# Optimization experiments

Hardware: AMD Instinct MI355X
Metric: run time of the kernel (lower is better)

Reference implementation:

```python
import jax, jax.numpy as jnp
import numpy as np

B, S, H, DH = 1, 4096, 8, 40  # hardcoded in the original forward
D = H * DH  # 320

def setup_inputs() -> dict:
    key = jax.random.key(0)
    ks = jax.random.split(key, 6)
    s = 1.0 / np.sqrt(D)
    return {
        "x": jax.random.normal(ks[0], (B, S, D), dtype=jnp.float32),
        "Wq": jax.random.normal(ks[1], (D, D), dtype=jnp.float32) * s,
        "Wk": jax.random.normal(ks[2], (D, D), dtype=jnp.float32) * s,
        "Wv": jax.random.normal(ks[3], (D, D), dtype=jnp.float32) * s,
        "Wo": jax.random.normal(ks[4], (D, D), dtype=jnp.float32) * s,
        "bo": jnp.zeros((D,), dtype=jnp.float32),
    }

def reference(x, Wq, Wk, Wv, Wo, bo):
    scale = DH ** (-0.5)
    # nn.Linear(bias=False): y = x @ W^T. context = x (self-attention).
    q = x @ Wq.T
    k = x @ Wk.T
    v = x @ Wv.T
    # split heads: [B,S,D] -> [B*H, S, DH]
    def split_heads(t):
        return t.reshape(B, S, H, DH).transpose(0, 2, 1, 3).reshape(B * H, S, DH)
    q, k, v = split_heads(q), split_heads(k), split_heads(v)
    # fp32 QK^T (original forces float), softmax, AV
    sim = jnp.einsum('bid,bjd->bij', q.astype(jnp.float32), k.astype(jnp.float32)) * scale
    attn = jax.nn.softmax(sim, axis=-1)
    out = jnp.einsum('bij,bjd->bid', attn, v)
    # merge heads: [B*H, S, DH] -> [B, S, D]
    out = out.reshape(B, H, S, DH).transpose(0, 2, 1, 3).reshape(B, S, D)
    return out @ Wo.T + bo
```

## Files before the change

### kernel.cpp

```cpp
#include <hip/hip_runtime.h>
#include <math.h>


#define NS 4096
#define ND 320
#define SCALE2 0.2281101152f
#define HS48 196608
#define VTH 163840
#define XN 1310720

typedef __attribute__((ext_vector_type(8))) short bf16x8;
typedef __attribute__((ext_vector_type(16))) float f32x16;

static __device__ __forceinline__ unsigned short f2bru(float f) {
  return (unsigned short)((__builtin_bit_cast(unsigned int, f) + 0x8000u) >> 16);
}
static __device__ __forceinline__ unsigned int pk2ru(float a, float b) {
  unsigned int ua = __builtin_bit_cast(unsigned int, a) + 0x8000u;
  unsigned int ub = __builtin_bit_cast(unsigned int, b) + 0x8000u;
  return __builtin_amdgcn_perm(ub, ua, 0x07060302u);
}
static __device__ __forceinline__ unsigned int pk2t(float a, float b) {
  return __builtin_amdgcn_perm(__builtin_bit_cast(unsigned int, b),
                               __builtin_bit_cast(unsigned int, a), 0x07060302u);
}
static __device__ __forceinline__ float fexp2(float x) {
  return __builtin_amdgcn_exp2f(x);
}
static __device__ __forceinline__ bf16x8 ld8(const unsigned short* p) {
  union { uint2 u[2]; bf16x8 v; } c;
  c.u[0] = *(const uint2*)p;
  c.u[1] = *(const uint2*)(p + 4);
  return c.v;
}
static __device__ __forceinline__ uint4 ld16u(const unsigned short* p) {
  uint2 a = *(const uint2*)p, b = *(const uint2*)(p + 4);
  return make_uint4(a.x, a.y, b.x, b.y);
}
static __device__ __forceinline__ void st16(unsigned short* p, uint4 v) {
  *(uint2*)p = make_uint2(v.x, v.y);
  *(uint2*)(p + 4) = make_uint2(v.z, v.w);
}
static __device__ __forceinline__ int sig32(int q) {
  int s = q >> 4, h2 = (q >> 3) & 1, j = q & 7;
  return (s << 4) | ((j >> 2) << 3) | (h2 << 2) | (j & 3);
}

__global__ __launch_bounds__(256) void proj_qkv_kernel(
    const float* __restrict__ x, const float* __restrict__ Wq,
    const float* __restrict__ Wk, const float* __restrict__ Wv,
    unsigned short* __restrict__ Qp, unsigned short* __restrict__ Kp,
    unsigned short* __restrict__ Vt) {
  const int zi = blockIdx.y;
  const int z = zi / 5;
  const int bnn = (zi - z * 5) * 64;
  const float* W = (z == 0) ? Wq : (z == 1) ? Wk : Wv;
  __shared__ __align__(16) unsigned short As[128 * 76];
  __shared__ __align__(16) unsigned short Bs[64 * 76];
  const int t = threadIdx.x;
  const int w = t >> 6, l = t & 63, l31 = l & 31, hi = l >> 5;
  const int bm = blockIdx.x * 128;
  const int m0 = w * 32;
  f32x16 acc0 = {0,0,0,0,0,0,0,0,0,0,0,0,0,0,0,0};
  f32x16 acc1 = {0,0,0,0,0,0,0,0,0,0,0,0,0,0,0,0};
  const unsigned short* af = As + (m0 + l31) * 76 + hi * 8;
  const unsigned short* bf0 = Bs + l31 * 76 + hi * 8;
  const unsigned short* bf1 = Bs + (32 + l31) * 76 + hi * 8;
  for (int k0 = 0; k0 < ND; k0 += 64) {
    __syncthreads();
#pragma unroll
    for (int i = 0; i < 4; i++) {
      int c = t + i * 256;
      int row = c >> 3, kc = (c & 7) << 3;
      const float* g = x + (bm + row) * ND + k0 + kc;
      float4 v0 = *(const float4*)g, v1 = *(const float4*)(g + 4);
      st16(As + row * 76 + kc,
           make_uint4(pk2ru(v0.x, v0.y), pk2ru(v0.z, v0.w),
                      pk2ru(v1.x, v1.y), pk2ru(v1.z, v1.w)));
    }
#pragma unroll
    for (int i = 0; i < 2; i++) {
      int c = t + i * 256;
      int row = c >> 3, kc = (c & 7) << 3;
      const float* g = W + (bnn + row) * ND + k0 + kc;
      float4 v0 = *(const float4*)g, v1 = *(const float4*)(g + 4);
      st16(Bs + row * 76 + kc,
           make_uint4(pk2ru(v0.x, v0.y), pk2ru(v0.z, v0.w),
                      pk2ru(v1.x, v1.y), pk2ru(v1.z, v1.w)));
    }
    __syncthreads();
#pragma unroll
    for (int ks = 0; ks < 4; ks++) {
      bf16x8 A = ld8(af + ks * 16);
      acc0 = __builtin_amdgcn_mfma_f32_32x32x16_bf16(A, ld8(bf0 + ks * 16), acc0, 0, 0, 0);
      acc1 = __builtin_amdgcn_mfma_f32_32x32x16_bf16(A, ld8(bf1 + ks * 16), acc1, 0, 0, 0);
    }
  }
  __syncthreads();
  if (z < 2) {
    unsigned short* Tile = As;
    unsigned short* Y = (z == 0) ? Qp : Kp;
    const float sc = (z == 0) ? SCALE2 : 1.0f;
    const unsigned int padw = (z == 0) ? 0xC200u : 0x3F80u;
#pragma unroll
    for (int r2 = 0; r2 < 16; r2++) {
      int lr = m0 + (r2 & 3) + 8 * (r2 >> 2) + 4 * hi;
      Tile[lr * 68 + l31] = f2bru(acc0[r2] * sc);
      Tile[lr * 68 + 32 + l31] = f2bru(acc1[r2] * sc);
    }
    __syncthreads();
#pragma unroll
    for (int i = 0; i < 4; i++) {
      int c = t + i * 256;
      int row = c >> 3, ch = c & 7;
      int j = bnn + ch * 8;
      int h = j / 40, dh = j - h * 40;
      uint4 v = ld16u(Tile + row * 68 + ch * 8);
      st16(Y + h * HS48 + (bm + row) * 48 + dh, v);
      if (dh == 0)
        st16(Y + h * HS48 + (bm + row) * 48 + 40, make_uint4(padw, 0u, 0u, 0u));
    }
  } else {
    unsigned short* Tile = As;
#pragma unroll
    for (int r2 = 0; r2 < 16; r2++) {
      int lr = m0 + (r2 & 3) + 8 * (r2 >> 2) + 4 * hi;
      Tile[l31 * 132 + lr] = f2bru(acc0[r2]);
      Tile[(32 + l31) * 132 + lr] = f2bru(acc1[r2]);
    }
    __syncthreads();
#pragma unroll
    for (int i = 0; i < 4; i++) {
      int c = t + i * 256;
      int row = c >> 4, ch = c & 15;
      int j = bnn + row;
      int h = j / 40, dd = j - h * 40;
      uint4 v = ld16u(Tile + row * 132 + ch * 8);
      st16(Vt + h * VTH + dd * NS + bm + ch * 8, v);
    }
  }
}

__global__ __launch_bounds__(256) void attn_kernel(
    const unsigned short* __restrict__ Qp, const unsigned short* __restrict__ Kp,
    const unsigned short* __restrict__ Vt, unsigned short* __restrict__ Op,
    float* __restrict__ Lp) {
  const int b = blockIdx.x;
  const int h = b & 7, ks = (b >> 3) & 7, qt = b >> 6;
  const int t = threadIdx.x;
  const int w = t >> 6, l = t & 63, l31 = l & 31, hi = l >> 5;
  __shared__ __align__(16) unsigned short Ks[64 * 68];
  __shared__ __align__(16) unsigned short Vs[48 * 68];
  for (int i = t; i < 272; i += 256)
    ((unsigned int*)(Vs + 40 * 68))[i] = (i < 34) ? 0x3F803F80u : 0u;

  const int kbase = ks * 512;
  const int qbase = qt * 128 + w * 32;
  const unsigned short* qp = Qp + h * HS48 + (qbase + l31) * 48 + hi * 8;
  bf16x8 qf0 = *(const bf16x8*)qp;
  bf16x8 qf1 = *(const bf16x8*)(qp + 16);
  bf16x8 qf2 = *(const bf16x8*)(qp + 32);

  f32x16 oa0 = {0,0,0,0,0,0,0,0,0,0,0,0,0,0,0,0};
  f32x16 oa1 = {0,0,0,0,0,0,0,0,0,0,0,0,0,0,0,0};

  const int kr0 = t / 6, kc0 = t - kr0 * 6;
  const int kr1 = (t + 256) / 6, kc1 = (t + 256) - kr1 * 6;
  const unsigned short* gK0 = Kp + h * HS48 + (kbase + kr0) * 48 + kc0 * 8;
  const unsigned short* gK1 = Kp + h * HS48 + (kbase + kr1) * 48 + kc1 * 8;
  unsigned short* lK0 = Ks + ((kr0 & 32) | sig32(kr0 & 31)) * 68 + kc0 * 8;
  unsigned short* lK1 = Ks + ((kr1 & 32) | sig32(kr1 & 31)) * 68 + kc1 * 8;
  const int vr0 = t >> 3, vc = t & 7, vr1 = 32 + vr0;
  const unsigned short* gV0 = Vt + h * VTH + vr0 * NS + kbase + vc * 8;
  const unsigned short* gV1 = Vt + h * VTH + vr1 * NS + kbase + vc * 8;
  unsigned short* lV0 = Vs + vr0 * 68 + vc * 8;
  unsigned short* lV1 = Vs + vr1 * 68 + vc * 8;

  const unsigned short* kf0 = Ks + l31 * 68 + hi * 8;
  const unsigned short* kf1 = Ks + (32 + l31) * 68 + hi * 8;
  const unsigned short* vf0 = Vs + l31 * 68 + hi * 8;
  const unsigned short* vf1 = Vs + (32 + (l31 & 15)) * 68 + hi * 8;

  uint4 ka = *(const uint4*)gK0;
  uint4 kb2, vb2;
  uint4 va = *(const uint4*)gV0;
  if (t < 128) kb2 = *(const uint4*)gK1;
  if (t < 64)  vb2 = *(const uint4*)gV1;

  for (int it = 0; it < 8; ++it) {
    __syncthreads();
    st16(lK0, ka);
    if (t < 128) st16(lK1, kb2);
    st16(lV0, va);
    if (t < 64) st16(lV1, vb2);
    __syncthreads();
    gK0 += 64 * 48; gK1 += 64 * 48; gV0 += 64; gV1 += 64;
    ka = *(const uint4*)gK0;
    va = *(const uint4*)gV0;
    if (t < 128) kb2 = *(const uint4*)gK1;
    if (t < 64)  vb2 = *(const uint4*)gV1;

    {
      f32x16 s0 = {0,0,0,0,0,0,0,0,0,0,0,0,0,0,0,0};
      s0 = __builtin_amdgcn_mfma_f32_32x32x16_bf16(ld8(kf0), qf0, s0, 0, 0, 0);
      s0 = __builtin_amdgcn_mfma_f32_32x32x16_bf16(ld8(kf0 + 16), qf1, s0, 0, 0, 0);
      s0 = __builtin_amdgcn_mfma_f32_32x32x16_bf16(ld8(kf0 + 32), qf2, s0, 0, 0, 0);
      unsigned int pw[8];
#pragma unroll
      for (int i = 0; i < 8; i++)
        pw[i] = pk2t(fexp2(s0[2 * i]), fexp2(s0[2 * i + 1]));
      bf16x8 pf0 = __builtin_bit_cast(bf16x8, make_uint4(pw[0], pw[1], pw[2], pw[3]));
      bf16x8 pf1 = __builtin_bit_cast(bf16x8, make_uint4(pw[4], pw[5], pw[6], pw[7]));
      oa0 = __builtin_amdgcn_mfma_f32_32x32x16_bf16(pf0, ld8(vf0), oa0, 0, 0, 0);
      oa1 = __builtin_amdgcn_mfma_f32_32x32x16_bf16(pf0, ld8(vf1), oa1, 0, 0, 0);
      oa0 = __builtin_amdgcn_mfma_f32_32x32x16_bf16(pf1, ld8(vf0 + 16), oa0, 0, 0, 0);
      oa1 = __builtin_amdgcn_mfma_f32_32x32x16_bf16(pf1, ld8(vf1 + 16), oa1, 0, 0, 0);
    }
    {
      f32x16 s1 = {0,0,0,0,0,0,0,0,0,0,0,0,0,0,0,0};
      s1 = __builtin_amdgcn_mfma_f32_32x32x16_bf16(ld8(kf1), qf0, s1, 0, 0, 0);
      s1 = __builtin_amdgcn_mfma_f32_32x32x16_bf16(ld8(kf1 + 16), qf1, s1, 0, 0, 0);
      s1 = __builtin_amdgcn_mfma_f32_32x32x16_bf16(ld8(kf1 + 32), qf2, s1, 0, 0, 0);
      unsigned int pw[8];
#pragma unroll
      for (int i = 0; i < 8; i++)
        pw[i] = pk2t(fexp2(s1[2 * i]), fexp2(s1[2 * i + 1]));
      bf16x8 pf2 = __builtin_bit_cast(bf16x8, make_uint4(pw[0], pw[1], pw[2], pw[3]));
      bf16x8 pf3 = __builtin_bit_cast(bf16x8, make_uint4(pw[4], pw[5], pw[6], pw[7]));
      oa0 = __builtin_amdgcn_mfma_f32_32x32x16_bf16(pf2, ld8(vf0 + 32), oa0, 0, 0, 0);
      oa1 = __builtin_amdgcn_mfma_f32_32x32x16_bf16(pf2, ld8(vf1 + 32), oa1, 0, 0, 0);
      oa0 = __builtin_amdgcn_mfma_f32_32x32x16_bf16(pf3, ld8(vf0 + 48), oa0, 0, 0, 0);
      oa1 = __builtin_amdgcn_mfma_f32_32x32x16_bf16(pf3, ld8(vf1 + 48), oa1, 0, 0, 0);
    }
  }

  unsigned short* opb = Op + ks * XN + h * 163840;
  float* lpb = Lp + ks * 32768 + h * NS;
#pragma unroll
  for (int r2 = 0; r2 < 16; r2++) {
    int qr = qbase + (r2 & 3) + 8 * (r2 >> 2) + 4 * hi;
    opb[qr * 40 + l31] = f2bru(oa0[r2]);
    if (l31 < 8) opb[qr * 40 + 32 + l31] = f2bru(oa1[r2]);
    if (l31 == 8) lpb[qr] = oa1[r2];
  }
}

__global__ __launch_bounds__(256) void combine_kernel(
    const unsigned short* __restrict__ Op, const float* __restrict__ Lp,
    unsigned short* __restrict__ Xo) {
  int e = (blockIdx.x * 256 + threadIdx.x) * 2;
  int h = e / 163840;
  int r = e - h * 163840;
  int s = r / 40;
  int dh = r - s * 40;
  float a0 = 0.f, a1 = 0.f, lsum = 0.f;
#pragma unroll
  for (int k = 0; k < 8; k++) {
    unsigned int u = *(const unsigned int*)(Op + k * XN + e);
    a0 += __builtin_bit_cast(float, u << 16);
    a1 += __builtin_bit_cast(float, u & 0xFFFF0000u);
    lsum += Lp[k * 32768 + h * NS + s];
  }
  float inv = 1.0f / lsum;
  *(unsigned int*)(Xo + s * ND + h * 40 + dh) = pk2ru(a0 * inv, a1 * inv);
}

__global__ __launch_bounds__(256) void proj_out_kernel(
    const unsigned short* __restrict__ Xo, const float* __restrict__ Wo,
    const float* __restrict__ bo, float* __restrict__ out) {
  __shared__ __align__(16) unsigned short As[128 * 76];
  __shared__ __align__(16) unsigned short Bs[64 * 76];
  const int t = threadIdx.x;
  const int w = t >> 6, l = t & 63, l31 = l & 31, hi = l >> 5;
  const int bm = blockIdx.x * 128;
  const int bnn = blockIdx.y * 64;
  const int m0 = w * 32;
  f32x16 acc0 = {0,0,0,0,0,0,0,0,0,0,0,0,0,0,0,0};
  f32x16 acc1 = {0,0,0,0,0,0,0,0,0,0,0,0,0,0,0,0};
  const unsigned short* af = As + (m0 + l31) * 76 + hi * 8;
  const unsigned short* bf0 = Bs + l31 * 76 + hi * 8;
  const unsigned short* bf1 = Bs + (32 + l31) * 76 + hi * 8;
  for (int k0 = 0; k0 < ND; k0 += 64) {
    __syncthreads();
#pragma unroll
    for (int i = 0; i < 4; i++) {
      int c = t + i * 256;
      int row = c >> 3, kc = (c & 7) << 3;
      uint4 v = *(const uint4*)(Xo + (bm + row) * ND + k0 + kc);
      st16(As + row * 76 + kc, v);
    }
#pragma unroll
    for (int i = 0; i < 2; i++) {
      int c = t + i * 256;
      int row = c >> 3, kc = (c & 7) << 3;
      const float* g = Wo + (bnn + row) * ND + k0 + kc;
      float4 v0 = *(const float4*)g, v1 = *(const float4*)(g + 4);
      st16(Bs + row * 76 + kc,
           make_uint4(pk2ru(v0.x, v0.y), pk2ru(v0.z, v0.w),
                      pk2ru(v1.x, v1.y), pk2ru(v1.z, v1.w)));
    }
    __syncthreads();
#pragma unroll
    for (int ks = 0; ks < 4; ks++) {
      bf16x8 A = ld8(af + ks * 16);
      acc0 = __builtin_amdgcn_mfma_f32_32x32x16_bf16(A, ld8(bf0 + ks * 16), acc0, 0, 0, 0);
      acc1 = __builtin_amdgcn_mfma_f32_32x32x16_bf16(A, ld8(bf1 + ks * 16), acc1, 0, 0, 0);
    }
  }
  const int j0 = bnn + l31, j1 = bnn + 32 + l31;
  const float bj0 = bo[j0], bj1 = bo[j1];
#pragma unroll
  for (int r2 = 0; r2 < 16; r2++) {
    int row = bm + m0 + (r2 & 3) + 8 * (r2 >> 2) + 4 * hi;
    out[row * ND + j0] = acc0[r2] + bj0;
    out[row * ND + j1] = acc1[r2] + bj1;
  }
}

extern "C" void kernel_launch(void* const* d_in, const int* in_sizes, int n_in,
                              void* d_out, int out_size, void* d_ws, size_t ws_size,
                              hipStream_t stream) {
  (void)in_sizes; (void)n_in; (void)out_size; (void)ws_size;
  const float* x  = (const float*)d_in[0];
  const float* Wq = (const float*)d_in[1];
  const float* Wk = (const float*)d_in[2];
  const float* Wv = (const float*)d_in[3];
  const float* Wo = (const float*)d_in[4];
  const float* bo = (const float*)d_in[5];
  float* out = (float*)d_out;

  unsigned short* Qp = (unsigned short*)d_ws;
  unsigned short* Kp = Qp + 8 * HS48;
  unsigned short* Vt = Kp + 8 * HS48;
  unsigned short* Xo = Vt + 8 * VTH;
  unsigned short* Op = Xo + XN;
  float* Lp = (float*)(Op + 8 * XN);

  proj_qkv_kernel<<<dim3(32, 15), 256, 0, stream>>>(x, Wq, Wk, Wv, Qp, Kp, Vt);
  attn_kernel<<<dim3(2048), 256, 0, stream>>>(Qp, Kp, Vt, Op, Lp);
  combine_kernel<<<dim3(2560), 256, 0, stream>>>(Op, Lp, Xo);
  proj_out_kernel<<<dim3(32, 5), 256, 0, stream>>>(Xo, Wo, bo, out);
}
```

Baseline: 131.7 us.

## Fuse split-K combine into attention kernel via last-block atomic tickets

Removes the separate combine kernel. Each attention block bumps an atomic ticket for its (query tile, head) after writing its partial output and row sums. The eighth block to finish reduces all partials for that tile and writes the normalized bf16 result. This saves a kernel launch and lets the reduction overlap with other attention blocks, at the cost of a threadfence, an atomic, a memset of the ticket array, and a serial tail on the last block.

```diff
diff --git a/kernel.cpp b/kernel.cpp
--- a/kernel.cpp
+++ b/kernel.cpp
@@ -41,7 +41,7 @@
   *(uint2*)p = make_uint2(v.x, v.y);
   *(uint2*)(p + 4) = make_uint2(v.z, v.w);
 }
-static __device__ __forceinline__ int sig32(int q) {
+static __device__ __forceinline__ int sig32v(int q) {
   int s = q >> 4, h2 = (q >> 3) & 1, j = q & 7;
   return (s << 4) | ((j >> 2) << 3) | (h2 << 2) | (j & 3);
 }
@@ -144,13 +144,15 @@
 __global__ __launch_bounds__(256) void attn_kernel(
     const unsigned short* __restrict__ Qp, const unsigned short* __restrict__ Kp,
     const unsigned short* __restrict__ Vt, unsigned short* __restrict__ Op,
-    float* __restrict__ Lp) {
+    float* __restrict__ Lp, unsigned short* __restrict__ Xo,
+    unsigned int* __restrict__ tickets) {
   const int b = blockIdx.x;
   const int h = b & 7, ks = (b >> 3) & 7, qt = b >> 6;
   const int t = threadIdx.x;
   const int w = t >> 6, l = t & 63, l31 = l & 31, hi = l >> 5;
   __shared__ __align__(16) unsigned short Ks[64 * 68];
   __shared__ __align__(16) unsigned short Vs[48 * 68];
+  __shared__ int sLast;
   for (int i = t; i < 272; i += 256)
     ((unsigned int*)(Vs + 40 * 68))[i] = (i < 34) ? 0x3F803F80u : 0u;
 
@@ -168,8 +170,8 @@
   const int kr1 = (t + 256) / 6, kc1 = (t + 256) - kr1 * 6;
   const unsigned short* gK0 = Kp + h * HS48 + (kbase + kr0) * 48 + kc0 * 8;
   const unsigned short* gK1 = Kp + h * HS48 + (kbase + kr1) * 48 + kc1 * 8;
-  unsigned short* lK0 = Ks + ((kr0 & 32) | sig32(kr0 & 31)) * 68 + kc0 * 8;
-  unsigned short* lK1 = Ks + ((kr1 & 32) | sig32(kr1 & 31)) * 68 + kc1 * 8;
+  unsigned short* lK0 = Ks + ((kr0 & 32) | sig32v(kr0 & 31)) * 68 + kc0 * 8;
+  unsigned short* lK1 = Ks + ((kr1 & 32) | sig32v(kr1 & 31)) * 68 + kc1 * 8;
   const int vr0 = t >> 3, vc = t & 7, vr1 = 32 + vr0;
   const unsigned short* gV0 = Vt + h * VTH + vr0 * NS + kbase + vc * 8;
   const unsigned short* gV1 = Vt + h * VTH + vr1 * NS + kbase + vc * 8;
@@ -243,26 +245,33 @@
     if (l31 < 8) opb[qr * 40 + 32 + l31] = f2bru(oa1[r2]);
     if (l31 == 8) lpb[qr] = oa1[r2];
   }
-}
-
-__global__ __launch_bounds__(256) void combine_kernel(
-    const unsigned short* __restrict__ Op, const float* __restrict__ Lp,
-    unsigned short* __restrict__ Xo) {
-  int e = (blockIdx.x * 256 + threadIdx.x) * 2;
-  int h = e / 163840;
-  int r = e - h * 163840;
-  int s = r / 40;
-  int dh = r - s * 40;
-  float a0 = 0.f, a1 = 0.f, lsum = 0.f;
-#pragma unroll
-  for (int k = 0; k < 8; k++) {
-    unsigned int u = *(const unsigned int*)(Op + k * XN + e);
-    a0 += __builtin_bit_cast(float, u << 16);
-    a1 += __builtin_bit_cast(float, u & 0xFFFF0000u);
-    lsum += Lp[k * 32768 + h * NS + s];
-  }
-  float inv = 1.0f / lsum;
-  *(unsigned int*)(Xo + s * ND + h * 40 + dh) = pk2ru(a0 * inv, a1 * inv);
+
+  __threadfence();
+  if (t == 0) {
+    unsigned int old = __hip_atomic_fetch_add(&tickets[(qt << 3) | h], 1u,
+                                              __ATOMIC_ACQ_REL,
+                                              __HIP_MEMORY_SCOPE_AGENT);
+    sLast = (old == 7);
+  }
+  __syncthreads();
+  if (sLast) {
+    const int qb0 = qt * 128;
+    for (int i = t; i < 2560; i += 256) {
+      int qi = i / 20, du = i - qi * 20;
+      int q = qb0 + qi;
+      float a0 = 0.f, a1 = 0.f, ls = 0.f;
+#pragma unroll
+      for (int k = 0; k < 8; k++) {
+        unsigned int uo =
+            *(const unsigned int*)(Op + k * XN + h * 163840 + q * 40 + du * 2);
+        a0 += __builtin_bit_cast(float, uo << 16);
+        a1 += __builtin_bit_cast(float, uo & 0xFFFF0000u);
+        ls += Lp[k * 32768 + h * NS + q];
+      }
+      float inv = 1.0f / ls;
+      *(unsigned int*)(Xo + q * ND + h * 40 + du * 2) = pk2ru(a0 * inv, a1 * inv);
+    }
+  }
 }
 
 __global__ __launch_bounds__(256) void proj_out_kernel(
@@ -335,9 +344,10 @@
   unsigned short* Xo = Vt + 8 * VTH;
   unsigned short* Op = Xo + XN;
   float* Lp = (float*)(Op + 8 * XN);
-
+  unsigned int* tickets = (unsigned int*)(Lp + 8 * 32768);
+
+  hipMemsetAsync(tickets, 0, 1024, stream);
   proj_qkv_kernel<<<dim3(32, 15), 256, 0, stream>>>(x, Wq, Wk, Wv, Qp, Kp, Vt);
-  attn_kernel<<<dim3(2048), 256, 0, stream>>>(Qp, Kp, Vt, Op, Lp);
-  combine_kernel<<<dim3(2560), 256, 0, stream>>>(Op, Lp, Xo);
+  attn_kernel<<<dim3(2048), 256, 0, stream>>>(Qp, Kp, Vt, Op, Lp, Xo, tickets);
   proj_out_kernel<<<dim3(32, 5), 256, 0, stream>>>(Xo, Wo, bo, out);
 }
```

Result: slower. 434.3 us (+229.8%).
